# Performance work log

Hardware: AMD Instinct MI355X
Metric: run time of the kernel (lower is better)

## Reference

```python
import jax, jax.numpy as jnp
import numpy as np

BATCH, SEQ, DIM, NUM_CODES = 8, 2048, 1024, 8192

def setup_inputs() -> dict:
    key = jax.random.key(0)
    kx, kc = jax.random.split(key)
    x = jax.random.normal(kx, (BATCH, SEQ, DIM), dtype=jnp.float32)
    # nn.Embedding default init: N(0, 1)
    codebook = jax.random.normal(kc, (NUM_CODES, DIM), dtype=jnp.float32)
    return {"x": x, "codebook": codebook}

def reference(x, codebook):
    # tau=0 path of CodebookLayer.forward (SnapFunction.forward):
    # similarity logits [B, S, num_codes], nearest-code argmax, gather.
    logits = jnp.einsum('bsd,cd->bsc', x, codebook)
    codebook_ids = jnp.argmax(logits, axis=-1)            # [B, S] int
    output = jnp.take(codebook, codebook_ids, axis=0)     # [B, S, D]
    return output
```

## Files before the change

kernel.cpp:

```cpp
#include <hip/hip_runtime.h>
#include <stdint.h>


#define T_TOKENS 16384
#define N_CODES  8192
#define DIM      1024
#define BM 256
#define BN 256
#define BK 64
#define NBLK (N_CODES / BM)
#define KITERS (DIM / BK)
#define EPS 13.0f
#define MAXCAND 48

typedef int   int8v  __attribute__((ext_vector_type(8)));
typedef int   int4v  __attribute__((ext_vector_type(4)));
typedef float f32x16 __attribute__((ext_vector_type(16)));

#define GLD16(gp, lp) \
  __builtin_amdgcn_global_load_lds((__attribute__((address_space(1))) void*)(gp), \
                                   (__attribute__((address_space(3))) void*)(lp), 16, 0, 0)

__device__ inline uint32_t umax(uint32_t a, uint32_t b) { return a > b ? a : b; }
__device__ inline uint32_t umin(uint32_t a, uint32_t b) { return a < b ? a : b; }
__device__ inline uint32_t umed3(uint32_t a, uint32_t b, uint32_t c) {
  return umax(umin(a, b), umin(umax(a, b), c));
}

__device__ inline uint32_t f32_key(float v) {
  int32_t b = (int32_t)__float_as_uint(v);
  return (uint32_t)(b ^ ((b >> 31) | (int32_t)0x80000000));
}
__device__ inline float key_f32(uint32_t u) {
  uint32_t b = (u & 0x80000000u) ? (u & 0x7FFFFFFFu) : ~u;
  return __uint_as_float(b);
}

__global__ __launch_bounds__(256) void vq_prep(const float* __restrict__ x,
                                               const float* __restrict__ cbm,
                                               uint8_t* __restrict__ xq,
                                               uint8_t* __restrict__ cq) {
  size_t b = blockIdx.x;
  const float* src; uint8_t* dst;
  if (b < 16384) { src = x;  dst = xq; }
  else           { b -= 16384; src = cbm; dst = cq; }
  const size_t i = b * 256 + threadIdx.x;
  const float4 v = ((const float4*)src)[i];
  uint32_t r = __builtin_amdgcn_cvt_pk_fp8_f32(v.x, v.y, 0, false);
  r = __builtin_amdgcn_cvt_pk_fp8_f32(v.z, v.w, (int)r, true);
  ((uint32_t*)dst)[i] = r;
}

#define MFMA8(A_, B_, C_) \
  __builtin_amdgcn_mfma_scale_f32_32x32x64_f8f6f4((A_), (B_), (C_), 0, 0, 0, \
                                                  0x7F7F7F7F, 0, 0x7F7F7F7F)

__global__ __launch_bounds__(256, 1) void vq_gemm_top3(
    const uint8_t* __restrict__ cq,
    const uint8_t* __restrict__ xq,
    uint32_t* __restrict__ pk)
{
  __shared__ uint8_t smem[4 * 32768];

  const int t    = threadIdx.x;
  const int wave = t >> 6;
  const int lane = t & 63;
  const int col  = lane & 31;
  const int hi   = lane >> 5;
  const int wm   = wave >> 1;
  const int wn   = wave & 1;

  const int f   = blockIdx.x;
  const int swz = (f & 7) * 256 + (f >> 3);
  const int cyi = swz >> 6;
  const int tb0 = (swz & 63) * BN;
  const int cb0 = cyi * BM;

  const int r0 = t >> 2;
  const int js = ((t & 3) ^ ((r0 >> 1) & 3)) * 16;
  const uint8_t* sA = cq + (size_t)(cb0 + r0) * DIM + js;
  const uint8_t* sB = xq + (size_t)(tb0 + r0) * DIM + js;

#define STAGE(bi, ti) do {                                           \
    uint8_t* Ad_ = smem + ((bi) << 15);                              \
    const int ko_ = (ti) * BK;                                       \
    GLD16(sA + ko_,                 Ad_ + t * 16);                   \
    GLD16(sA + 64 * DIM + ko_,      Ad_ + t * 16 + 4096);            \
    GLD16(sA + 128 * DIM + ko_,     Ad_ + t * 16 + 8192);            \
    GLD16(sA + 192 * DIM + ko_,     Ad_ + t * 16 + 12288);           \
    GLD16(sB + ko_,                 Ad_ + 16384 + t * 16);           \
    GLD16(sB + 64 * DIM + ko_,      Ad_ + 16384 + t * 16 + 4096);    \
    GLD16(sB + 128 * DIM + ko_,     Ad_ + 16384 + t * 16 + 8192);    \
    GLD16(sB + 192 * DIM + ko_,     Ad_ + 16384 + t * 16 + 12288);   \
  } while (0)

  const int j0 = hi * 2;
  int aoff[4][2], boff[4][2];
#pragma unroll
  for (int mi = 0; mi < 4; ++mi) {
    const int ra = wm * 128 + mi * 32 + col;
    const int pa = (ra >> 1) & 3;
    aoff[mi][0] = ra * 64 + (j0 ^ pa) * 16;
    aoff[mi][1] = ra * 64 + ((j0 + 1) ^ pa) * 16;
    const int rb = wn * 128 + mi * 32 + col;
    const int pb = (rb >> 1) & 3;
    boff[mi][0] = 16384 + rb * 64 + (j0 ^ pb) * 16;
    boff[mi][1] = 16384 + rb * 64 + ((j0 + 1) ^ pb) * 16;
  }

#define READ8(dst_, o0_, o1_) do {                                         \
    const int4v lo_ = *(const int4v*)(cur + (o0_));                        \
    const int4v hq_ = *(const int4v*)(cur + (o1_));                        \
    dst_ = __builtin_shufflevector(lo_, hq_, 0, 1, 2, 3, 4, 5, 6, 7);      \
  } while (0)

  f32x16 acc[4][4];
#pragma unroll
  for (int i = 0; i < 4; ++i)
#pragma unroll
    for (int j = 0; j < 4; ++j)
#pragma unroll
      for (int r = 0; r < 16; ++r) acc[i][j][r] = 0.f;

  STAGE(0, 0);
  STAGE(1, 1);

#pragma unroll
  for (int kt = 0; kt < KITERS; ++kt) {
    if (kt == KITERS - 1) asm volatile("s_waitcnt vmcnt(0)" ::: "memory");
    else                  asm volatile("s_waitcnt vmcnt(8)" ::: "memory");
    __builtin_amdgcn_s_barrier();
    __builtin_amdgcn_sched_barrier(0);

    const uint8_t* cur = smem + ((kt & 3) << 15);

    if (kt < KITERS - 2) STAGE((kt + 2) & 3, kt + 2);

    int8v b[4];
#pragma unroll
    for (int nj = 0; nj < 4; ++nj) READ8(b[nj], boff[nj][0], boff[nj][1]);
#pragma unroll
    for (int mi = 0; mi < 4; ++mi) {
      int8v a;
      READ8(a, aoff[mi][0], aoff[mi][1]);
      acc[mi][0] = MFMA8(a, b[0], acc[mi][0]);
      acc[mi][1] = MFMA8(a, b[1], acc[mi][1]);
      acc[mi][2] = MFMA8(a, b[2], acc[mi][2]);
      acc[mi][3] = MFMA8(a, b[3], acc[mi][3]);
    }
  }
  __syncthreads();

  uint32_t* cand = (uint32_t*)smem;
  const int invb = 255 - wm * 128 - 4 * hi;
#pragma unroll
  for (int nj = 0; nj < 4; ++nj) {
    uint32_t K1 = 0, K2 = 0, K3 = 0;
#pragma unroll
    for (int mi = 0; mi < 4; ++mi) {
#pragma unroll
      for (int rg = 0; rg < 16; ++rg) {
        const int rowoff = (rg & 3) + 8 * (rg >> 2);
        const uint32_t key = (f32_key(acc[mi][nj][rg]) & 0xFFFFFF00u)
                           | (uint32_t)(invb - mi * 32 - rowoff);
        const uint32_t t3 = umed3(key, K2, K3);
        const uint32_t t2 = umed3(key, K1, K2);
        K1 = umax(key, K1); K2 = t2; K3 = t3;
      }
    }
    const uint32_t o1 = __shfl_xor(K1, 32, 64);
    const uint32_t o2 = __shfl_xor(K2, 32, 64);
    const uint32_t o3 = __shfl_xor(K3, 32, 64);
    const uint32_t m1 = umin(K1, o1), M2 = umax(K2, o2);
    const uint32_t m2 = umin(K2, o2), M3 = umax(K3, o3);
    K1 = umax(K1, o1);
    const uint32_t nk2 = umax(m1, M2);
    K3 = umax(umax(m2, umin(m1, M2)), M3);
    K2 = nk2;
    if (hi == 0) {
      uint32_t* c = &cand[((wn * 128 + nj * 32 + col) * 2 + wm) * 3];
      c[0] = K1; c[1] = K2; c[2] = K3;
    }
  }
  __syncthreads();
  {
    const uint32_t a1 = cand[(t * 2 + 0) * 3 + 0], a2 = cand[(t * 2 + 0) * 3 + 1],
                   a3 = cand[(t * 2 + 0) * 3 + 2];
    const uint32_t b1k = cand[(t * 2 + 1) * 3 + 0], b2 = cand[(t * 2 + 1) * 3 + 1],
                   b3 = cand[(t * 2 + 1) * 3 + 2];
    const uint32_t m1 = umin(a1, b1k), M2 = umax(a2, b2);
    const uint32_t m2 = umin(a2, b2), M3 = umax(a3, b3);
    uint32_t* dst = pk + ((size_t)(tb0 + t) * NBLK + cyi) * 3;
    dst[0] = umax(a1, b1k);
    dst[1] = umax(m1, M2);
    dst[2] = umax(umax(m2, umin(m1, M2)), M3);
  }
#undef STAGE
#undef READ8
}

__global__ __launch_bounds__(256) void vq_reduce_gather(
    const uint32_t* __restrict__ pk, const float* __restrict__ x,
    const float* __restrict__ cb, float* __restrict__ out)
{
  __shared__ float xs[DIM];
  __shared__ uint32_t wmax[4];
  __shared__ int scand[MAXCAND];
  __shared__ int scnt;
  __shared__ double sdot[MAXCAND];
  __shared__ int sbesti;

  const int tkn = blockIdx.x, t = threadIdx.x, lane = t & 63, wv = t >> 6;
  ((float4*)xs)[t] = ((const float4*)(x + (size_t)tkn * DIM))[t];
  const uint32_t key = (t < 3 * NBLK) ? pk[(size_t)tkn * (3 * NBLK) + t] : 0u;
  uint32_t m = key;
#pragma unroll
  for (int d = 1; d < 64; d <<= 1) m = umax(m, __shfl_xor(m, d, 64));
  if (t == 0) scnt = 0;
  if (lane == 0) wmax[wv] = m;
  __syncthreads();
  const float Mv = key_f32(umax(umax(wmax[0], wmax[1]), umax(wmax[2], wmax[3])));
  if (t < 3 * NBLK && key_f32(key) >= Mv - EPS) {
    const int p = atomicAdd(&scnt, 1);
    if (p < MAXCAND) scand[p] = (t / 3) * BM + 255 - (int)(key & 255u);
  }
  __syncthreads();
  const int cnt = scnt < MAXCAND ? scnt : MAXCAND;

  if (cnt > 1) {
    for (int k = wv; k < cnt; k += 4) {
      const int c = scand[k];
      const float* cr = cb + (size_t)c * DIM;
      double s = 0.0;
#pragma unroll
      for (int q = 0; q < 4; ++q) {
        const float4 xv = ((const float4*)xs)[lane + 64 * q];
        const float4 cv = ((const float4*)cr)[lane + 64 * q];
        s += (double)xv.x * cv.x + (double)xv.y * cv.y
           + (double)xv.z * cv.z + (double)xv.w * cv.w;
      }
#pragma unroll
      for (int d = 1; d < 64; d <<= 1) s += __shfl_xor(s, d, 64);
      if (lane == 0) sdot[k] = s;
    }
    __syncthreads();
    if (t == 0) {
      double best = -1e300; int bi = N_CODES;
      for (int k = 0; k < cnt; ++k) {
        const int c = scand[k];
        if (sdot[k] > best || (sdot[k] == best && c < bi)) { best = sdot[k]; bi = c; }
      }
      sbesti = bi;
    }
  } else {
    if (t == 0) sbesti = scand[0];
  }
  __syncthreads();
  const int code = sbesti;
  ((float4*)(out + (size_t)tkn * DIM))[t] = ((const float4*)(cb + (size_t)code * DIM))[t];
}

__global__ __launch_bounds__(256) void vq_naive(const float* __restrict__ x,
                                                const float* __restrict__ cb,
                                                float* __restrict__ out) {
  __shared__ float xs[DIM];
  __shared__ float bv[256];
  __shared__ int   bix[256];
  const int tkn = blockIdx.x;
  const int t = threadIdx.x;
  for (int d = t; d < DIM; d += 256) xs[d] = x[(size_t)tkn * DIM + d];
  __syncthreads();
  float best = -1e30f; int bi = N_CODES;
  for (int c = t; c < N_CODES; c += 256) {
    const float* cr = cb + (size_t)c * DIM;
    float s = 0.f;
    for (int d = 0; d < DIM; ++d) s += xs[d] * cr[d];
    if (s > best || (s == best && c < bi)) { best = s; bi = c; }
  }
  bv[t] = best; bix[t] = bi;
  __syncthreads();
  for (int off = 128; off > 0; off >>= 1) {
    if (t < off) {
      if (bv[t + off] > bv[t] || (bv[t + off] == bv[t] && bix[t + off] < bix[t])) {
        bv[t] = bv[t + off]; bix[t] = bix[t + off];
      }
    }
    __syncthreads();
  }
  const int code = bix[0];
  for (int d = t; d < DIM; d += 256)
    out[(size_t)tkn * DIM + d] = cb[(size_t)code * DIM + d];
}

extern "C" void kernel_launch(void* const* d_in, const int* in_sizes, int n_in,
                              void* d_out, int out_size, void* d_ws, size_t ws_size,
                              hipStream_t stream) {
  const float* x  = (const float*)d_in[0];
  const float* cb = (const float*)d_in[1];
  float* out = (float*)d_out;

  const size_t MB = 1024 * 1024;
  const size_t need = 24 * MB + (size_t)T_TOKENS * NBLK * 3 * 4;
  if (ws_size >= need) {
    uint8_t*  xq = (uint8_t*)d_ws;
    uint8_t*  cq = xq + 16 * MB;
    uint32_t* pk = (uint32_t*)(cq + 8 * MB);

    vq_prep<<<dim3(24576), 256, 0, stream>>>(x, cb, xq, cq);
    vq_gemm_top3<<<dim3((T_TOKENS / BN) * (N_CODES / BM)), 256, 0, stream>>>(cq, xq, pk);
    vq_reduce_gather<<<dim3(T_TOKENS), 256, 0, stream>>>(pk, x, cb, out);
  } else {
    vq_naive<<<dim3(T_TOKENS), 256, 0, stream>>>(x, cb, out);
  }
}
```

Measured before the change: 340.6 us.

## Software-pipeline LDS fragment reads with register double-buffering and triple LDS buffers

Restructures the FP8 GEMM main loop so the LDS-to-register reads for iteration k+1 are issued before the MFMAs of iteration k. Fragments are double-buffered in registers, and the LDS ring drops from four stages to three, with global loads issued three tiles ahead. The aim is to hide LDS read latency behind MFMA work and to cut shared memory use. The cost is extra VGPRs for the second fragment set, plus tighter wait/barrier ordering that must stay correct with three buffers.

```diff
diff --git a/kernel.cpp b/kernel.cpp
--- a/kernel.cpp
+++ b/kernel.cpp
@@ -60,7 +60,7 @@
     const uint8_t* __restrict__ xq,
     uint32_t* __restrict__ pk)
 {
-  __shared__ uint8_t smem[4 * 32768];
+  __shared__ uint8_t smem[3 * 32768];
 
   const int t    = threadIdx.x;
   const int wave = t >> 6;
@@ -82,7 +82,7 @@
   const uint8_t* sB = xq + (size_t)(tb0 + r0) * DIM + js;
 
 #define STAGE(bi, ti) do {                                           \
-    uint8_t* Ad_ = smem + ((bi) << 15);                              \
+    uint8_t* Ad_ = smem + (bi) * 32768;                              \
     const int ko_ = (ti) * BK;                                       \
     GLD16(sA + ko_,                 Ad_ + t * 16);                   \
     GLD16(sA + 64 * DIM + ko_,      Ad_ + t * 16 + 4096);            \
@@ -114,39 +114,55 @@
     dst_ = __builtin_shufflevector(lo_, hq_, 0, 1, 2, 3, 4, 5, 6, 7);      \
   } while (0)
 
+#define READFRAGS(set_, bufi_) do {                                        \
+    const uint8_t* cur = smem + (bufi_) * 32768;                           \
+    READ8(bf[set_][0], boff[0][0], boff[0][1]);                            \
+    READ8(bf[set_][1], boff[1][0], boff[1][1]);                            \
+    READ8(bf[set_][2], boff[2][0], boff[2][1]);                            \
+    READ8(bf[set_][3], boff[3][0], boff[3][1]);                            \
+    READ8(af[set_][0], aoff[0][0], aoff[0][1]);                            \
+    READ8(af[set_][1], aoff[1][0], aoff[1][1]);                            \
+    READ8(af[set_][2], aoff[2][0], aoff[2][1]);                            \
+    READ8(af[set_][3], aoff[3][0], aoff[3][1]);                            \
+  } while (0)
+
   f32x16 acc[4][4];
 #pragma unroll
-  for (int i = 0; i < 4; ++i)
-#pragma unroll
-    for (int j = 0; j < 4; ++j)
-#pragma unroll
-      for (int r = 0; r < 16; ++r) acc[i][j][r] = 0.f;
+  for (int i2 = 0; i2 < 4; ++i2)
+#pragma unroll
+    for (int j2 = 0; j2 < 4; ++j2)
+#pragma unroll
+      for (int r = 0; r < 16; ++r) acc[i2][j2][r] = 0.f;
+
+  int8v af[2][4], bf[2][4];
 
   STAGE(0, 0);
   STAGE(1, 1);
+  asm volatile("s_waitcnt vmcnt(8)" ::: "memory");
+  __builtin_amdgcn_s_barrier();
+  __builtin_amdgcn_sched_barrier(0);
+  READFRAGS(0, 0);
+  STAGE(2, 2);
 
 #pragma unroll
   for (int kt = 0; kt < KITERS; ++kt) {
-    if (kt == KITERS - 1) asm volatile("s_waitcnt vmcnt(0)" ::: "memory");
-    else                  asm volatile("s_waitcnt vmcnt(8)" ::: "memory");
+    const int cs = kt & 1, ns = cs ^ 1;
+    if (kt <= 13) asm volatile("s_waitcnt lgkmcnt(0) vmcnt(8)" ::: "memory");
+    else          asm volatile("s_waitcnt lgkmcnt(0) vmcnt(0)" ::: "memory");
     __builtin_amdgcn_s_barrier();
     __builtin_amdgcn_sched_barrier(0);
 
-    const uint8_t* cur = smem + ((kt & 3) << 15);
-
-    if (kt < KITERS - 2) STAGE((kt + 2) & 3, kt + 2);
-
-    int8v b[4];
-#pragma unroll
-    for (int nj = 0; nj < 4; ++nj) READ8(b[nj], boff[nj][0], boff[nj][1]);
+    if (kt <= 12) STAGE((kt + 3) % 3, kt + 3);
+
+    if (kt <= 14) READFRAGS(ns, (kt + 1) % 3);
+    __builtin_amdgcn_sched_barrier(0);
+
 #pragma unroll
     for (int mi = 0; mi < 4; ++mi) {
-      int8v a;
-      READ8(a, aoff[mi][0], aoff[mi][1]);
-      acc[mi][0] = MFMA8(a, b[0], acc[mi][0]);
-      acc[mi][1] = MFMA8(a, b[1], acc[mi][1]);
-      acc[mi][2] = MFMA8(a, b[2], acc[mi][2]);
-      acc[mi][3] = MFMA8(a, b[3], acc[mi][3]);
+      acc[mi][0] = MFMA8(af[cs][mi], bf[cs][0], acc[mi][0]);
+      acc[mi][1] = MFMA8(af[cs][mi], bf[cs][1], acc[mi][1]);
+      acc[mi][2] = MFMA8(af[cs][mi], bf[cs][2], acc[mi][2]);
+      acc[mi][3] = MFMA8(af[cs][mi], bf[cs][3], acc[mi][3]);
     }
   }
   __syncthreads();
@@ -197,6 +213,7 @@
   }
 #undef STAGE
 #undef READ8
+#undef READFRAGS
 }
 
 __global__ __launch_bounds__(256) void vq_reduce_gather(
```

After: 354.5 us. 1.04x slower.
